# Performance work log

Hardware: AMD Instinct MI355X
Metric: run time of the kernel (lower is better)

The kernel has to match this reference:

```python
import jax, jax.numpy as jnp
import numpy as np

N_NODES = 50000
N_EDGES = 800000
IN_DIM = 8
HID = 32
HEADS = 4
D1 = HID * HEADS  # 128


def setup_inputs() -> dict:
    key = jax.random.key(0)
    ks = jax.random.split(key, 10)
    x = jax.random.normal(ks[0], (N_NODES, IN_DIM), dtype=jnp.float32)
    edge_index = jax.random.randint(ks[1], (2, N_EDGES), 0, N_NODES, dtype=jnp.int64)
    s = lambda fan_in: 1.0 / np.sqrt(fan_in)
    W1 = jax.random.uniform(ks[2], (IN_DIM, D1), jnp.float32, -s(IN_DIM), s(IN_DIM))
    a1 = jax.random.uniform(ks[3], (2 * D1, 1), jnp.float32, -s(2 * D1), s(2 * D1))
    W2 = jax.random.uniform(ks[4], (D1, HID), jnp.float32, -s(D1), s(D1))
    a2 = jax.random.uniform(ks[5], (2 * HID, 1), jnp.float32, -s(2 * HID), s(2 * HID))
    hw1 = jax.random.uniform(ks[6], (HID, 32), jnp.float32, -s(HID), s(HID))
    hb1 = jax.random.uniform(ks[7], (32,), jnp.float32, -s(HID), s(HID))
    hw2 = jax.random.uniform(ks[8], (32, 1), jnp.float32, -s(32), s(32))
    hb2 = jax.random.uniform(ks[9], (1,), jnp.float32, -s(32), s(32))
    return {"x": x, "edge_index": edge_index, "W1": W1, "a1": a1,
            "W2": W2, "a2": a2, "hw1": hw1, "hb1": hb1, "hw2": hw2, "hb2": hb2}


def gat_layer(h, src, dst, W, a, n_nodes):
    # Wh: [N, D]; attention vector split so logits are computed per-node then gathered
    Wh = h @ W
    D = Wh.shape[-1]
    a_src, a_dst = a[:D, 0], a[D:, 0]
    # alpha = LeakyReLU([Wh[src] || Wh[dst]] @ a)  (same math, no [E, 2D] concat)
    alpha = jax.nn.leaky_relu((Wh @ a_src)[src] + (Wh @ a_dst)[dst], negative_slope=0.2)
    alpha_exp = jnp.exp(alpha - alpha.max())  # global-max shift, as in the original
    alpha_sum = jax.ops.segment_sum(alpha_exp, dst, num_segments=n_nodes)
    alpha_norm = alpha_exp / (alpha_sum[dst] + 1e-9)
    out = jax.ops.segment_sum(alpha_norm[:, None] * Wh[src], dst, num_segments=n_nodes)
    return jax.nn.elu(out), alpha_norm


def reference(x, edge_index, W1, a1, W2, a2, hw1, hb1, hw2, hb2):
    src, dst = edge_index[0], edge_index[1]
    n = x.shape[0]
    h, _ = gat_layer(x, src, dst, W1, a1, n)
    h, _ = gat_layer(h, src, dst, W2, a2, n)
    # head: Linear -> GELU -> (Dropout: identity in eval) -> Linear
    z = jax.nn.gelu(h @ hw1 + hb1, approximate=False)
    node_scores = (z @ hw2 + hb2).squeeze(-1)
    return node_scores
```

## Files before the change

### kernel.cpp

```cpp
#include <hip/hip_runtime.h>
#include <math.h>

#define N_NODES 50000
#define IN_DIM 8
#define HID 32
#define D1 128

#define CAP 64

#define FG 8
#define FB 128
#define GRANGE (N_NODES / FG)
#define FILL_BLOCKS (FG * FB)
#define SD1_BLOCKS ((N_NODES + 255) / 256)

__global__ void k_fill_sd1(const int* __restrict__ src, const int* __restrict__ dst,
                           int* __restrict__ cnt, int* __restrict__ esrc,
                           const float* __restrict__ x, const float* __restrict__ W1,
                           const float* __restrict__ a1,
                           float* __restrict__ px, float* __restrict__ d1,
                           int n_edges) {
    __shared__ float bs[IN_DIM], bd[IN_DIM];
    const int t = threadIdx.x;
    if (blockIdx.x < FILL_BLOCKS) {
        const int g = blockIdx.x & (FG - 1);
        const int blk = blockIdx.x >> 3;
        const int lo = g * GRANGE, hi = lo + GRANGE;
        const int base = blk * blockDim.x + t;
        const int step = FB * blockDim.x;
        for (int i = base; i * 4 < n_edges; i += step) {
            const int4 d4 = *(const int4*)&dst[i * 4];
            const bool mx = d4.x >= lo && d4.x < hi;
            const bool my = d4.y >= lo && d4.y < hi;
            const bool mz = d4.z >= lo && d4.z < hi;
            const bool mw = d4.w >= lo && d4.w < hi;
            if (mx | my | mz | mw) {
                const int4 s4 = *(const int4*)&src[i * 4];
                if (mx) { const int p = atomicAdd(&cnt[d4.x], 1); if (p < CAP) esrc[d4.x * CAP + p] = s4.x; }
                if (my) { const int p = atomicAdd(&cnt[d4.y], 1); if (p < CAP) esrc[d4.y * CAP + p] = s4.y; }
                if (mz) { const int p = atomicAdd(&cnt[d4.z], 1); if (p < CAP) esrc[d4.z * CAP + p] = s4.z; }
                if (mw) { const int p = atomicAdd(&cnt[d4.w], 1); if (p < CAP) esrc[d4.w * CAP + p] = s4.w; }
            }
        }
    } else {
        if (t < 16) {
            const int k = t & 7;
            const float* av = a1 + ((t < 8) ? 0 : D1);
            float acc = 0.f;
            for (int j = 0; j < D1; ++j) acc += W1[k * D1 + j] * av[j];
            if (t < 8) bs[k] = acc; else bd[k] = acc;
        }
        __syncthreads();
        const int node = (blockIdx.x - FILL_BLOCKS) * blockDim.x + t;
        if (node >= N_NODES) return;
        const float4 x0 = *(const float4*)&x[node * 8];
        const float4 x1 = *(const float4*)&x[node * 8 + 4];
        const float s1v = x0.x*bs[0] + x0.y*bs[1] + x0.z*bs[2] + x0.w*bs[3]
                        + x1.x*bs[4] + x1.y*bs[5] + x1.z*bs[6] + x1.w*bs[7];
        d1[node]       = x0.x*bd[0] + x0.y*bd[1] + x0.z*bd[2] + x0.w*bd[3]
                        + x1.x*bd[4] + x1.y*bd[5] + x1.z*bd[6] + x1.w*bd[7];
        *(float4*)&px[node * 16]     = x0;
        *(float4*)&px[node * 16 + 4] = x1;
        px[node * 16 + 8] = s1v;
    }
}

__global__ void k_aggr_mid(const int* __restrict__ esrc, const int* __restrict__ cnt,
                           const float* __restrict__ px, const float* __restrict__ d,
                           const float* __restrict__ W1, const float* __restrict__ W2,
                           const float* __restrict__ a2,
                           float* __restrict__ Wh2,
                           float* __restrict__ s2, float* __restrict__ d2) {
    __shared__ float xa_s[8][IN_DIM];
    __shared__ float h_s[8][D1];
    const int t = threadIdx.x;
    const int wv = t >> 6;
    const int lane = t & 63;
    const int half = lane >> 5, sub = lane & 31;
    const int nodeBase = blockIdx.x * 8;
    const int node = nodeBase + wv * 2 + half;
    const int start = node * CAP;
    const int deg = cnt[node];
    const float dn = d[node];
    float4 aLo = {0.f, 0.f, 0.f, 0.f};
    float4 aHi = {0.f, 0.f, 0.f, 0.f};
    float wsum = 0.f;
    for (int idx = sub; idx < deg; idx += 32) {
        const int se = esrc[start + idx];
        const float4 v0 = *(const float4*)&px[se * 16];
        const float4 v1 = *(const float4*)&px[se * 16 + 4];
        const float sv = px[se * 16 + 8];
        float a = sv + dn;
        a = a > 0.f ? a : 0.2f * a;
        const float ww = expf(a);
        aLo.x += ww * v0.x;  aLo.y += ww * v0.y;
        aLo.z += ww * v0.z;  aLo.w += ww * v0.w;
        aHi.x += ww * v1.x;  aHi.y += ww * v1.y;
        aHi.z += ww * v1.z;  aHi.w += ww * v1.w;
        wsum += ww;
    }
#pragma unroll
    for (int off = 1; off < 32; off <<= 1) {
        aLo.x += __shfl_xor(aLo.x, off);
        aLo.y += __shfl_xor(aLo.y, off);
        aLo.z += __shfl_xor(aLo.z, off);
        aLo.w += __shfl_xor(aLo.w, off);
        aHi.x += __shfl_xor(aHi.x, off);
        aHi.y += __shfl_xor(aHi.y, off);
        aHi.z += __shfl_xor(aHi.z, off);
        aHi.w += __shfl_xor(aHi.w, off);
        wsum  += __shfl_xor(wsum, off);
    }
    const float inv = 1.f / (wsum + 1e-9f);
    if (sub == 0) {
        float4 o; o.x = aLo.x*inv; o.y = aLo.y*inv; o.z = aLo.z*inv; o.w = aLo.w*inv;
        *(float4*)&xa_s[wv * 2 + half][0] = o;
    } else if (sub == 1) {
        float4 o; o.x = aHi.x*inv; o.y = aHi.y*inv; o.z = aHi.z*inv; o.w = aHi.w*inv;
        *(float4*)&xa_s[wv * 2 + half][4] = o;
    }
    __syncthreads();
    const int nloc = t >> 5;
    const int col = t & 31;
    const float xa0 = xa_s[nloc][0], xa1 = xa_s[nloc][1];
    const float xa2 = xa_s[nloc][2], xa3 = xa_s[nloc][3];
    const float xa4 = xa_s[nloc][4], xa5 = xa_s[nloc][5];
    const float xa6 = xa_s[nloc][6], xa7 = xa_s[nloc][7];
#pragma unroll
    for (int j = 0; j < 4; ++j) {
        const int k = col + 32 * j;
        float h = xa0 * W1[0 * D1 + k] + xa1 * W1[1 * D1 + k]
                + xa2 * W1[2 * D1 + k] + xa3 * W1[3 * D1 + k]
                + xa4 * W1[4 * D1 + k] + xa5 * W1[5 * D1 + k]
                + xa6 * W1[6 * D1 + k] + xa7 * W1[7 * D1 + k];
        h_s[nloc][k] = h > 0.f ? h : (expf(h) - 1.f);
    }
    __syncthreads();
    float o = 0.f;
#pragma unroll 8
    for (int k = 0; k < D1; ++k) o += h_s[nloc][k] * W2[k * HID + col];
    float ss = o * a2[col];
    float dd = o * a2[HID + col];
#pragma unroll
    for (int off = 1; off < 32; off <<= 1) {
        ss += __shfl_xor(ss, off);
        dd += __shfl_xor(dd, off);
    }
    const int node2 = nodeBase + nloc;
    Wh2[node2 * HID + col] = o;
    if (col == 0) { s2[node2] = ss; d2[node2] = dd; }
}

__global__ void k_aggr32_head(const int* __restrict__ esrc, const int* __restrict__ cnt,
                              const float* __restrict__ s, const float* __restrict__ d,
                              const float* __restrict__ Wh,
                              const float* __restrict__ hw1, const float* __restrict__ hb1,
                              const float* __restrict__ hw2, const float* __restrict__ hb2,
                              float* __restrict__ scores) {
    const int w = (blockIdx.x * blockDim.x + threadIdx.x) >> 6;
    const int lane = threadIdx.x & 63;
    const int half = lane >> 5, sub = lane & 31, base = lane & 32;
    const int node = w * 2 + half;
    if (node >= N_NODES) return;
    const int start = node * CAP;
    const int deg = cnt[node];
    const float dn = d[node];
    const int slot = sub >> 3;
    const int cp = sub & 7;
    float4 acc = {0.f, 0.f, 0.f, 0.f};
    float wsum = 0.f;
    for (int idx = slot; idx < deg; idx += 4) {
        const int se = esrc[start + idx];
        float a = s[se] + dn;
        a = a > 0.f ? a : 0.2f * a;
        const float ww = expf(a);
        const float4 v = *(const float4*)&Wh[se * HID + cp * 4];
        acc.x += ww * v.x;  acc.y += ww * v.y;
        acc.z += ww * v.z;  acc.w += ww * v.w;
        wsum += ww;
    }
#pragma unroll
    for (int off = 8; off < 32; off <<= 1) {
        acc.x += __shfl_xor(acc.x, off);
        acc.y += __shfl_xor(acc.y, off);
        acc.z += __shfl_xor(acc.z, off);
        acc.w += __shfl_xor(acc.w, off);
        wsum  += __shfl_xor(wsum, off);
    }
    const float inv = 1.f / (wsum + 1e-9f);
    acc.x *= inv;  acc.y *= inv;  acc.z *= inv;  acc.w *= inv;
    const int srcl = base + (sub >> 2);
    const float g0 = __shfl(acc.x, srcl);
    const float g1 = __shfl(acc.y, srcl);
    const float g2 = __shfl(acc.z, srcl);
    const float g3 = __shfl(acc.w, srcl);
    const int r = sub & 3;
    float v = (r == 0) ? g0 : (r == 1) ? g1 : (r == 2) ? g2 : g3;
    const float h = v > 0.f ? v : (expf(v) - 1.f);
    float z = hb1[sub];
#pragma unroll
    for (int k = 0; k < HID; ++k) {
        const float hk = __shfl(h, base + k);
        z += hk * hw1[k * HID + sub];
    }
    z = 0.5f * z * (1.f + erff(z * 0.7071067811865475f));
    float sc = z * hw2[sub];
#pragma unroll
    for (int off = 16; off > 0; off >>= 1) sc += __shfl_xor(sc, off);
    if (sub == 0) scores[node] = sc + hb2[0];
}

extern "C" void kernel_launch(void* const* d_in, const int* in_sizes, int n_in,
                              void* d_out, int out_size, void* d_ws, size_t ws_size,
                              hipStream_t stream) {
    const float* x   = (const float*)d_in[0];
    const int*   ei  = (const int*)d_in[1];
    const float* W1  = (const float*)d_in[2];
    const float* a1  = (const float*)d_in[3];
    const float* W2  = (const float*)d_in[4];
    const float* a2  = (const float*)d_in[5];
    const float* hw1 = (const float*)d_in[6];
    const float* hb1 = (const float*)d_in[7];
    const float* hw2 = (const float*)d_in[8];
    const float* hb2 = (const float*)d_in[9];
    float* out = (float*)d_out;

    const int n_edges = in_sizes[1] / 2;
    const int* src = ei;
    const int* dst = ei + n_edges;

    float* p = (float*)d_ws;
    float* px   = p; p += (size_t)N_NODES * 16;
    float* Wh2  = p; p += (size_t)N_NODES * HID;
    float* d1   = p; p += N_NODES;
    float* s2   = p; p += N_NODES;
    float* d2   = p; p += N_NODES;
    int* cnt    = (int*)p; p += N_NODES;
    int* esrc   = (int*)p; p += (size_t)N_NODES * CAP;

    hipMemsetAsync(cnt, 0, N_NODES * sizeof(int), stream);

    const int AGGR_BLOCKS = (N_NODES * 32 + 255) / 256;

    k_fill_sd1<<<FILL_BLOCKS + SD1_BLOCKS, 256, 0, stream>>>(
        src, dst, cnt, esrc, x, W1, a1, px, d1, n_edges);

    k_aggr_mid<<<(N_NODES + 7) / 8, 256, 0, stream>>>(esrc, cnt, px, d1,
                                                      W1, W2, a2, Wh2, s2, d2);

    k_aggr32_head<<<AGGR_BLOCKS, 256, 0, stream>>>(esrc, cnt, s2, d2, Wh2,
                                                   hw1, hb1, hw2, hb2, out);
}
```

Measured before the change: 180.9 us.

## Process 32 nodes per block with 8 lanes per node in mid aggregation

```diff
diff --git a/kernel.cpp b/kernel.cpp
--- a/kernel.cpp
+++ b/kernel.cpp
@@ -71,36 +71,39 @@
                            const float* __restrict__ a2,
                            float* __restrict__ Wh2,
                            float* __restrict__ s2, float* __restrict__ d2) {
-    __shared__ float xa_s[8][IN_DIM];
-    __shared__ float h_s[8][D1];
+    __shared__ float xa_s[32][IN_DIM];
+    __shared__ float h_s[32][132];
     const int t = threadIdx.x;
     const int wv = t >> 6;
     const int lane = t & 63;
-    const int half = lane >> 5, sub = lane & 31;
-    const int nodeBase = blockIdx.x * 8;
-    const int node = nodeBase + wv * 2 + half;
-    const int start = node * CAP;
-    const int deg = cnt[node];
-    const float dn = d[node];
+    const int nodeBase = blockIdx.x * 32;
+    const int nl = lane >> 3;
+    const int sub8 = lane & 7;
+    const int node = nodeBase + wv * 8 + nl;
     float4 aLo = {0.f, 0.f, 0.f, 0.f};
     float4 aHi = {0.f, 0.f, 0.f, 0.f};
     float wsum = 0.f;
-    for (int idx = sub; idx < deg; idx += 32) {
-        const int se = esrc[start + idx];
-        const float4 v0 = *(const float4*)&px[se * 16];
-        const float4 v1 = *(const float4*)&px[se * 16 + 4];
-        const float sv = px[se * 16 + 8];
-        float a = sv + dn;
-        a = a > 0.f ? a : 0.2f * a;
-        const float ww = expf(a);
-        aLo.x += ww * v0.x;  aLo.y += ww * v0.y;
-        aLo.z += ww * v0.z;  aLo.w += ww * v0.w;
-        aHi.x += ww * v1.x;  aHi.y += ww * v1.y;
-        aHi.z += ww * v1.z;  aHi.w += ww * v1.w;
-        wsum += ww;
-    }
-#pragma unroll
-    for (int off = 1; off < 32; off <<= 1) {
+    if (node < N_NODES) {
+        const int start = node * CAP;
+        const int deg = cnt[node];
+        const float dn = d[node];
+        for (int idx = sub8; idx < deg; idx += 8) {
+            const int se = esrc[start + idx];
+            const float4 v0 = *(const float4*)&px[se * 16];
+            const float4 v1 = *(const float4*)&px[se * 16 + 4];
+            const float sv = px[se * 16 + 8];
+            float a = sv + dn;
+            a = a > 0.f ? a : 0.2f * a;
+            const float ww = expf(a);
+            aLo.x += ww * v0.x;  aLo.y += ww * v0.y;
+            aLo.z += ww * v0.z;  aLo.w += ww * v0.w;
+            aHi.x += ww * v1.x;  aHi.y += ww * v1.y;
+            aHi.z += ww * v1.z;  aHi.w += ww * v1.w;
+            wsum += ww;
+        }
+    }
+#pragma unroll
+    for (int off = 1; off < 8; off <<= 1) {
         aLo.x += __shfl_xor(aLo.x, off);
         aLo.y += __shfl_xor(aLo.y, off);
         aLo.z += __shfl_xor(aLo.z, off);
@@ -112,23 +115,23 @@
         wsum  += __shfl_xor(wsum, off);
     }
     const float inv = 1.f / (wsum + 1e-9f);
-    if (sub == 0) {
+    if (sub8 == 0) {
         float4 o; o.x = aLo.x*inv; o.y = aLo.y*inv; o.z = aLo.z*inv; o.w = aLo.w*inv;
-        *(float4*)&xa_s[wv * 2 + half][0] = o;
-    } else if (sub == 1) {
+        *(float4*)&xa_s[wv * 8 + nl][0] = o;
+    } else if (sub8 == 1) {
         float4 o; o.x = aHi.x*inv; o.y = aHi.y*inv; o.z = aHi.z*inv; o.w = aHi.w*inv;
-        *(float4*)&xa_s[wv * 2 + half][4] = o;
+        *(float4*)&xa_s[wv * 8 + nl][4] = o;
     }
     __syncthreads();
-    const int nloc = t >> 5;
-    const int col = t & 31;
+    const int nloc = t >> 3;
+    const int l8 = t & 7;
     const float xa0 = xa_s[nloc][0], xa1 = xa_s[nloc][1];
     const float xa2 = xa_s[nloc][2], xa3 = xa_s[nloc][3];
     const float xa4 = xa_s[nloc][4], xa5 = xa_s[nloc][5];
     const float xa6 = xa_s[nloc][6], xa7 = xa_s[nloc][7];
 #pragma unroll
-    for (int j = 0; j < 4; ++j) {
-        const int k = col + 32 * j;
+    for (int j = 0; j < 16; ++j) {
+        const int k = l8 + 8 * j;
         float h = xa0 * W1[0 * D1 + k] + xa1 * W1[1 * D1 + k]
                 + xa2 * W1[2 * D1 + k] + xa3 * W1[3 * D1 + k]
                 + xa4 * W1[4 * D1 + k] + xa5 * W1[5 * D1 + k]
@@ -136,19 +139,32 @@
         h_s[nloc][k] = h > 0.f ? h : (expf(h) - 1.f);
     }
     __syncthreads();
-    float o = 0.f;
+    const int c0 = l8 * 4;
+    float4 o4 = {0.f, 0.f, 0.f, 0.f};
 #pragma unroll 8
-    for (int k = 0; k < D1; ++k) o += h_s[nloc][k] * W2[k * HID + col];
-    float ss = o * a2[col];
-    float dd = o * a2[HID + col];
-#pragma unroll
-    for (int off = 1; off < 32; off <<= 1) {
+    for (int k4 = 0; k4 < D1 / 4; ++k4) {
+        const float4 h4 = *(const float4*)&h_s[nloc][k4 * 4];
+        const float4 w0 = *(const float4*)&W2[(k4 * 4    ) * HID + c0];
+        const float4 w1 = *(const float4*)&W2[(k4 * 4 + 1) * HID + c0];
+        const float4 w2 = *(const float4*)&W2[(k4 * 4 + 2) * HID + c0];
+        const float4 w3 = *(const float4*)&W2[(k4 * 4 + 3) * HID + c0];
+        o4.x += h4.x*w0.x + h4.y*w1.x + h4.z*w2.x + h4.w*w3.x;
+        o4.y += h4.x*w0.y + h4.y*w1.y + h4.z*w2.y + h4.w*w3.y;
+        o4.z += h4.x*w0.z + h4.y*w1.z + h4.z*w2.z + h4.w*w3.z;
+        o4.w += h4.x*w0.w + h4.y*w1.w + h4.z*w2.w + h4.w*w3.w;
+    }
+    const int node2 = nodeBase + nloc;
+    float ss = o4.x*a2[c0] + o4.y*a2[c0+1] + o4.z*a2[c0+2] + o4.w*a2[c0+3];
+    float dd = o4.x*a2[HID+c0] + o4.y*a2[HID+c0+1] + o4.z*a2[HID+c0+2] + o4.w*a2[HID+c0+3];
+#pragma unroll
+    for (int off = 1; off < 8; off <<= 1) {
         ss += __shfl_xor(ss, off);
         dd += __shfl_xor(dd, off);
     }
-    const int node2 = nodeBase + nloc;
-    Wh2[node2 * HID + col] = o;
-    if (col == 0) { s2[node2] = ss; d2[node2] = dd; }
+    if (node2 < N_NODES) {
+        *(float4*)&Wh2[node2 * HID + c0] = o4;
+        if (l8 == 0) { s2[node2] = ss; d2[node2] = dd; }
+    }
 }
 
 __global__ void k_aggr32_head(const int* __restrict__ esrc, const int* __restrict__ cnt,
@@ -245,8 +261,8 @@
     k_fill_sd1<<<FILL_BLOCKS + SD1_BLOCKS, 256, 0, stream>>>(
         src, dst, cnt, esrc, x, W1, a1, px, d1, n_edges);
 
-    k_aggr_mid<<<(N_NODES + 7) / 8, 256, 0, stream>>>(esrc, cnt, px, d1,
-                                                      W1, W2, a2, Wh2, s2, d2);
+    k_aggr_mid<<<(N_NODES + 31) / 32, 256, 0, stream>>>(esrc, cnt, px, d1,
+                                                        W1, W2, a2, Wh2, s2, d2);
 
     k_aggr32_head<<<AGGR_BLOCKS, 256, 0, stream>>>(esrc, cnt, s2, d2, Wh2,
                                                    hw1, hb1, hw2, hb2, out);
```

Result: no change. 184.1 us (+1.8%).
